# Optimization experiments

Measured on AMD Instinct MI355X. Metric: run time of the kernel, lower is better.

## Reference

```python
import jax, jax.numpy as jnp
import numpy as np

B, T, C = 4, 2048, 768
H, D = 6, 128


def apply_rotary_emb(x, cos, sin):
    # x: (B, T, H, D); cos, sin: (1, T, 1, D//2)
    d = x.shape[-1] // 2
    x1, x2 = x[..., :d], x[..., d:]
    y1 = x1 * cos + x2 * sin
    y2 = -x1 * sin + x2 * cos
    return jnp.concatenate([y1, y2], axis=-1)


def rmsnorm(x):
    eps = 1e-15
    ms = jnp.mean(x * x, axis=-1, keepdims=True)
    return x / jnp.sqrt(ms + eps)


def setup_inputs() -> dict:
    key = jax.random.key(0)
    ks = jax.random.split(key, 7)
    s = 0.02
    return {
        "x": jax.random.normal(ks[0], (B, T, C), jnp.float32),
        "cos": jax.random.normal(ks[1], (1, T, 1, D // 2), jnp.float32),
        "sin": jax.random.normal(ks[2], (1, T, 1, D // 2), jnp.float32),
        "Wq": jax.random.normal(ks[3], (C, C), jnp.float32) * s,
        "Wk": jax.random.normal(ks[4], (C, C), jnp.float32) * s,
        "Wv": jax.random.normal(ks[5], (C, C), jnp.float32) * s,
        "Wo": jax.random.normal(ks[6], (C, C), jnp.float32) * s,
    }


def reference(x, cos, sin, Wq, Wk, Wv, Wo):
    b, t, c = x.shape
    # QKV projections (nn.Linear: x @ W.T)
    q = (x @ Wq.T).reshape(b, t, H, D)
    k = (x @ Wk.T).reshape(b, t, H, D)
    v = (x @ Wv.T).reshape(b, t, H, D)
    # RoPE then QK-RMSNorm
    q = rmsnorm(apply_rotary_emb(q, cos, sin))
    k = rmsnorm(apply_rotary_emb(k, cos, sin))
    # (B, H, T, D)
    q = q.transpose(0, 2, 1, 3)
    k = k.transpose(0, 2, 1, 3)
    v = v.transpose(0, 2, 1, 3)
    scores = jnp.einsum('bhqd,bhkd->bhqk', q, k) / jnp.sqrt(jnp.float32(D))
    causal = jnp.tril(jnp.ones((t, t), dtype=bool))
    scores = jnp.where(causal[None, None], scores, -jnp.inf)
    attn = jax.nn.softmax(scores, axis=-1)
    out = jnp.einsum('bhqk,bhkd->bhqd', attn, v)
    out = out.transpose(0, 2, 1, 3).reshape(b, t, c)
    return out @ Wo.T
```

## Files before the change

### kernel.cpp

```cpp
#include <hip/hip_runtime.h>

#define T_SEQ 2048
#define NH    6
#define HD    128
#define CDIM  768
#define NQKV  2304
#define MROWS 8192
#define NSLOT 1920

typedef __attribute__((ext_vector_type(8))) short bf16x8;
typedef __attribute__((ext_vector_type(4))) float f32x4;

__device__ __forceinline__ unsigned short f2bf(float f){
  unsigned int u = __builtin_bit_cast(unsigned int, f);
  u += 0x7fffu + ((u >> 16) & 1u);
  return (unsigned short)(u >> 16);
}
__device__ __forceinline__ float bf2f(unsigned short h){
  unsigned int u = ((unsigned int)h) << 16;
  return __builtin_bit_cast(float, u);
}

__device__ __forceinline__ void gload_lds16(const void* g, void* l){
  __builtin_amdgcn_global_load_lds(
      (const __attribute__((address_space(1))) unsigned int*)g,
      (__attribute__((address_space(3))) unsigned int*)l, 16, 0, 0);
}

__device__ __forceinline__ int offq(int q){
  return q < 8 ? q : q < 16 ? 8 + 2*(q-8) : q < 24 ? 24 + 3*(q-16) : 48 + 4*(q-24);
}

__global__ __launch_bounds__(256) void cvt_f32_bf16(
    const float* __restrict__ in, unsigned short* __restrict__ out, int n4){
  int i = blockIdx.x * 256 + threadIdx.x;
  if (i >= n4) return;
  float4 v = reinterpret_cast<const float4*>(in)[i];
  ushort4 o;
  o.x = f2bf(v.x); o.y = f2bf(v.y); o.z = f2bf(v.z); o.w = f2bf(v.w);
  reinterpret_cast<ushort4*>(out)[i] = o;
}

__global__ __launch_bounds__(256) void cvt_w4(
    const float* __restrict__ w0, const float* __restrict__ w1,
    const float* __restrict__ w2, const float* __restrict__ w3,
    unsigned short* __restrict__ out){
  const int which = blockIdx.y;
  const float* src = which == 0 ? w0 : which == 1 ? w1 : which == 2 ? w2 : w3;
  int i = blockIdx.x * 256 + threadIdx.x;
  float4 v = reinterpret_cast<const float4*>(src)[i];
  ushort4 o;
  o.x = f2bf(v.x); o.y = f2bf(v.y); o.z = f2bf(v.z); o.w = f2bf(v.w);
  reinterpret_cast<ushort4*>(out + (size_t)which * CDIM * CDIM)[i] = o;
}

template<int BF16OUT>
__global__ __launch_bounds__(256) void gemm_bt(
    const unsigned short* __restrict__ A,
    const unsigned short* __restrict__ B,
    void* __restrict__ Cv, int M, int N, int K)
{
  __shared__ unsigned short As[128 * 64];
  __shared__ unsigned short Bs[128 * 64];
  const int tid  = threadIdx.x;
  const int lane = tid & 63;
  const int wave = tid >> 6;
  const int wm = wave >> 1, wn = wave & 1;
  const int lr = lane & 15, lg = lane >> 4;
  const int srow = lane >> 3;
  const int sslot = (lane & 7) ^ (lane >> 3);
  const int row0 = blockIdx.x * 128, col0 = blockIdx.y * 128;

  f32x4 acc[4][4];
  const f32x4 z = {0.f, 0.f, 0.f, 0.f};
  #pragma unroll
  for (int i = 0; i < 4; ++i)
    #pragma unroll
    for (int j = 0; j < 4; ++j) acc[i][j] = z;

  for (int k0 = 0; k0 < K; k0 += 64){
    #pragma unroll
    for (int i = 0; i < 4; ++i){
      int seg = wave * 4 + i;
      int r = seg * 8 + srow;
      gload_lds16(&A[(size_t)(row0 + r) * K + k0 + sslot * 8], &As[seg * 512]);
      gload_lds16(&B[(size_t)(col0 + r) * K + k0 + sslot * 8], &Bs[seg * 512]);
    }
    __syncthreads();
    #pragma unroll
    for (int kk = 0; kk < 64; kk += 32){
      bf16x8 af[4], bfr[4];
      #pragma unroll
      for (int mi = 0; mi < 4; ++mi)
        af[mi] = *reinterpret_cast<const bf16x8*>(
            &As[(wm*64 + mi*16 + lr) * 64 + ((((kk>>3) + lg) ^ (lr & 7)) * 8)]);
      #pragma unroll
      for (int ni = 0; ni < 4; ++ni)
        bfr[ni] = *reinterpret_cast<const bf16x8*>(
            &Bs[(wn*64 + ni*16 + lr) * 64 + ((((kk>>3) + lg) ^ (lr & 7)) * 8)]);
      #pragma unroll
      for (int mi = 0; mi < 4; ++mi)
        #pragma unroll
        for (int ni = 0; ni < 4; ++ni)
          acc[mi][ni] = __builtin_amdgcn_mfma_f32_16x16x32_bf16(af[mi], bfr[ni], acc[mi][ni], 0, 0, 0);
    }
    __syncthreads();
  }
  #pragma unroll
  for (int mi = 0; mi < 4; ++mi){
    #pragma unroll
    for (int ni = 0; ni < 4; ++ni){
      #pragma unroll
      for (int r = 0; r < 4; ++r){
        int row = row0 + wm*64 + mi*16 + lg*4 + r;
        int col = col0 + wn*64 + ni*16 + lr;
        if (BF16OUT)
          reinterpret_cast<unsigned short*>(Cv)[(size_t)row * N + col] = f2bf(acc[mi][ni][r]);
        else
          reinterpret_cast<float*>(Cv)[(size_t)row * N + col] = acc[mi][ni][r];
      }
    }
  }
}

__global__ __launch_bounds__(256) void rope_rms(
    unsigned short* __restrict__ QKVb,
    const float* __restrict__ cosp, const float* __restrict__ sinp)
{
  const int bt    = blockIdx.x;
  const int task  = blockIdx.y * 4 + (threadIdx.x >> 6);
  const int which = task / NH;
  const int h     = task % NH;
  const int t     = bt & (T_SEQ - 1);
  const int lane  = threadIdx.x & 63;
  unsigned short* p = QKVb + (size_t)bt * NQKV + which * CDIM + h * HD;
  float x1 = bf2f(p[lane]);
  float x2 = bf2f(p[lane + 64]);
  float c = cosp[t * 64 + lane];
  float s = sinp[t * 64 + lane];
  float y1 = x1 * c + x2 * s;
  float y2 = x2 * c - x1 * s;
  float ss = y1 * y1 + y2 * y2;
  #pragma unroll
  for (int off = 1; off < 64; off <<= 1) ss += __shfl_xor(ss, off);
  float inv = rsqrtf(ss * (1.0f / 128.0f) + 1e-15f);
  p[lane]      = f2bf(y1 * inv);
  p[lane + 64] = f2bf(y2 * inv);
}

__global__ __launch_bounds__(256) void transpose_v(
    const unsigned short* __restrict__ QKVb, unsigned short* __restrict__ Vt)
{
  __shared__ unsigned short tile[64][66];
  const int tid = threadIdx.x;
  const int t0  = blockIdx.x * 64;
  const int hd  = blockIdx.y;
  const int b   = blockIdx.z;
  const int h = hd >> 1, dhalf = (hd & 1) * 64;
  const unsigned short* src = QKVb + (size_t)b * T_SEQ * NQKV + 2 * CDIM + h * HD + dhalf;
  #pragma unroll
  for (int it = 0; it < 2; ++it){
    int ch = tid + it * 256;
    int r = ch >> 3, cc = (ch & 7) * 8;
    *reinterpret_cast<int4*>(&tile[r][cc]) =
        *reinterpret_cast<const int4*>(&src[(size_t)(t0 + r) * NQKV + cc]);
  }
  __syncthreads();
  unsigned short* dst = Vt + ((size_t)(b * NH + h) * HD + dhalf) * T_SEQ + t0;
  #pragma unroll
  for (int it = 0; it < 2; ++it){
    int ch = tid + it * 256;
    int d = ch >> 3, cc = (ch & 7) * 8;
    union { int4 v; unsigned short u[8]; } w;
    #pragma unroll
    for (int j = 0; j < 8; ++j) w.u[j] = tile[cc + j][d];
    *reinterpret_cast<int4*>(&dst[(size_t)d * T_SEQ + cc]) = w.v;
  }
}

__global__ __launch_bounds__(256) void attn_fwd(
    const unsigned short* __restrict__ QKVb,
    const unsigned short* __restrict__ Vt,
    unsigned short* __restrict__ AO,
    float* __restrict__ Op, float* __restrict__ Mp, float* __restrict__ Lp,
    int split)
{
  __shared__ unsigned short Ks[64][136];
  __shared__ unsigned short Vs[128][72];
  const int tid = threadIdx.x;
  const int lane = tid & 63, wave = tid >> 6;
  const int lr = lane & 15, lg = lane >> 4;
  float* Ps = reinterpret_cast<float*>(&Ks[0][0]) + wave * 1024;

  const int bh = blockIdx.y;
  const int b = bh / NH, h = bh % NH;
  int q, c, nc;
  if (split){
    int L = blockIdx.x;
    if (L < 8)      { q = L; c = 0; }
    else if (L < 24){ int m = L - 8;  q = 8 + (m >> 1); c = m & 1; }
    else if (L < 48){ int m = L - 24; q = 16 + m / 3;   c = m % 3; }
    else            { int m = L - 48; q = 24 + (m >> 2); c = m & 3; }
    nc = (q + 8) >> 3;
  } else { q = blockIdx.x; c = 0; nc = 1; }
  const int q0 = q * 64;
  const int qw = q0 + wave * 16;
  const int tbeg = c * 8;
  const int tend = split ? ((tbeg + 8 < q + 1) ? tbeg + 8 : q + 1) : q + 1;

  const unsigned short* Qp = QKVb + (size_t)(b * T_SEQ) * NQKV + h * HD;
  const unsigned short* Kp = QKVb + (size_t)(b * T_SEQ) * NQKV + CDIM + h * HD;
  const unsigned short* Vp = Vt + (size_t)bh * HD * T_SEQ;

  bf16x8 qf[4];
  #pragma unroll
  for (int c4 = 0; c4 < 4; ++c4)
    qf[c4] = *reinterpret_cast<const bf16x8*>(&Qp[(size_t)(qw + lr) * NQKV + c4 * 32 + lg * 8]);

  const f32x4 z = {0.f, 0.f, 0.f, 0.f};
  f32x4 o[8];
  #pragma unroll
  for (int dt = 0; dt < 8; ++dt) o[dt] = z;
  float mrun[4], lrun[4];
  #pragma unroll
  for (int r = 0; r < 4; ++r){ mrun[r] = -__builtin_inff(); lrun[r] = 0.f; }
  const float scl = 0.08838834764831845f;

  for (int t = tbeg; t < tend; ++t){
    const int kv0 = t * 64;
    #pragma unroll
    for (int it = 0; it < 4; ++it){
      int ch = tid + it * 256;
      int r = ch >> 4, cc = (ch & 15) * 8;
      *reinterpret_cast<int4*>(&Ks[r][cc]) =
          *reinterpret_cast<const int4*>(&Kp[(size_t)(kv0 + r) * NQKV + cc]);
      int rv = ch >> 3, cv = (ch & 7) * 8;
      *reinterpret_cast<int4*>(&Vs[rv][cv]) =
          *reinterpret_cast<const int4*>(&Vp[(size_t)rv * T_SEQ + kv0 + cv]);
    }
    __syncthreads();

    f32x4 s[4];
    #pragma unroll
    for (int nt = 0; nt < 4; ++nt) s[nt] = z;
    __builtin_amdgcn_s_setprio(1);
    #pragma unroll
    for (int c4 = 0; c4 < 4; ++c4){
      #pragma unroll
      for (int nt = 0; nt < 4; ++nt){
        bf16x8 kf = *reinterpret_cast<const bf16x8*>(&Ks[nt * 16 + lr][c4 * 32 + lg * 8]);
        s[nt] = __builtin_amdgcn_mfma_f32_16x16x32_bf16(qf[c4], kf, s[nt], 0, 0, 0);
      }
    }
    __builtin_amdgcn_s_setprio(0);
    __syncthreads();

    if (kv0 + 63 > qw){
      #pragma unroll
      for (int nt = 0; nt < 4; ++nt){
        int kg = kv0 + nt * 16 + lr;
        #pragma unroll
        for (int r = 0; r < 4; ++r){
          int qg = qw + lg * 4 + r;
          s[nt][r] = (kg <= qg) ? s[nt][r] * scl : -__builtin_inff();
        }
      }
    } else {
      #pragma unroll
      for (int nt = 0; nt < 4; ++nt)
        #pragma unroll
        for (int r = 0; r < 4; ++r) s[nt][r] *= scl;
    }

    float pm[4], rs[4];
    #pragma unroll
    for (int r = 0; r < 4; ++r)
      pm[r] = fmaxf(fmaxf(s[0][r], s[1][r]), fmaxf(s[2][r], s[3][r]));
    #pragma unroll
    for (int off = 1; off < 16; off <<= 1){
      #pragma unroll
      for (int r = 0; r < 4; ++r) pm[r] = fmaxf(pm[r], __shfl_xor(pm[r], off));
    }
    bool grow = false;
    #pragma unroll
    for (int r = 0; r < 4; ++r) grow = grow || (pm[r] > mrun[r]);
    if (__any(grow)){
      float sc[4];
      #pragma unroll
      for (int r = 0; r < 4; ++r){
        float mn = fmaxf(mrun[r], pm[r]);
        sc[r] = (mrun[r] == -__builtin_inff()) ? 0.f : __expf(mrun[r] - mn);
        mrun[r] = mn;
      }
      #pragma unroll
      for (int r = 0; r < 4; ++r) lrun[r] *= sc[r];
      #pragma unroll
      for (int dt = 0; dt < 8; ++dt)
        #pragma unroll
        for (int r = 0; r < 4; ++r) o[dt][r] *= sc[r];
    }
    #pragma unroll
    for (int r = 0; r < 4; ++r) rs[r] = 0.f;
    #pragma unroll
    for (int nt = 0; nt < 4; ++nt)
      #pragma unroll
      for (int r = 0; r < 4; ++r){
        float p = __expf(s[nt][r] - mrun[r]);
        s[nt][r] = p;
        rs[r] += p;
      }
    #pragma unroll
    for (int off = 1; off < 16; off <<= 1){
      #pragma unroll
      for (int r = 0; r < 4; ++r) rs[r] += __shfl_xor(rs[r], off);
    }
    #pragma unroll
    for (int r = 0; r < 4; ++r) lrun[r] += rs[r];

    #pragma unroll
    for (int nt = 0; nt < 4; ++nt)
      #pragma unroll
      for (int r = 0; r < 4; ++r){
        int row = lg * 4 + r;
        Ps[row * 64 + ((nt * 16 + lr) ^ ((row & 7) << 2))] = s[nt][r];
      }

    __builtin_amdgcn_s_setprio(1);
    #pragma unroll
    for (int kc = 0; kc < 2; ++kc){
      float4 p0 = *reinterpret_cast<const float4*>(
          &Ps[lr * 64 + ((kc * 32 + lg * 8) ^ ((lr & 7) << 2))]);
      float4 p1 = *reinterpret_cast<const float4*>(
          &Ps[lr * 64 + (((kc * 32 + lg * 8) + 4) ^ ((lr & 7) << 2))]);
      union { bf16x8 v; unsigned short u[8]; } pa;
      pa.u[0] = f2bf(p0.x); pa.u[1] = f2bf(p0.y); pa.u[2] = f2bf(p0.z); pa.u[3] = f2bf(p0.w);
      pa.u[4] = f2bf(p1.x); pa.u[5] = f2bf(p1.y); pa.u[6] = f2bf(p1.z); pa.u[7] = f2bf(p1.w);
      #pragma unroll
      for (int dt = 0; dt < 8; ++dt){
        bf16x8 vf = *reinterpret_cast<const bf16x8*>(&Vs[dt * 16 + lr][kc * 32 + lg * 8]);
        o[dt] = __builtin_amdgcn_mfma_f32_16x16x32_bf16(pa.v, vf, o[dt], 0, 0, 0);
      }
    }
    __builtin_amdgcn_s_setprio(0);
    __syncthreads();
  }

  if (nc == 1){
    float inv[4];
    #pragma unroll
    for (int r = 0; r < 4; ++r) inv[r] = 1.0f / lrun[r];
    #pragma unroll
    for (int dt = 0; dt < 8; ++dt)
      #pragma unroll
      for (int r = 0; r < 4; ++r)
        AO[((size_t)b * T_SEQ + qw + lg * 4 + r) * CDIM + h * HD + dt * 16 + lr] =
            f2bf(o[dt][r] * inv[r]);
  } else {
    const int slot = bh * 80 + offq(q) + c;
    float* OpW = Op + (size_t)slot * 64 * 128;
    #pragma unroll
    for (int dt = 0; dt < 8; ++dt)
      #pragma unroll
      for (int r = 0; r < 4; ++r)
        OpW[(wave * 16 + lg * 4 + r) * 128 + dt * 16 + lr] = o[dt][r];
    if (lr == 0){
      #pragma unroll
      for (int r = 0; r < 4; ++r){
        int row = wave * 16 + lg * 4 + r;
        Mp[(size_t)slot * 64 + row] = mrun[r];
        Lp[(size_t)slot * 64 + row] = lrun[r];
      }
    }
  }
}

__global__ __launch_bounds__(256) void attn_combine(
    const float* __restrict__ Op, const float* __restrict__ Mp,
    const float* __restrict__ Lp, unsigned short* __restrict__ AO)
{
  const int q  = 8 + blockIdx.x;
  const int bh = blockIdx.y;
  const int b = bh / NH, h = bh % NH;
  const int nc = (q + 8) >> 3;
  const int slot0 = bh * 80 + offq(q);
  #pragma unroll
  for (int u = 0; u < 8; ++u){
    int unit = threadIdx.x + u * 256;
    int r = unit >> 5, d4 = unit & 31;
    float m = -__builtin_inff();
    for (int cc = 0; cc < nc; ++cc)
      m = fmaxf(m, Mp[(size_t)(slot0 + cc) * 64 + r]);
    float l = 0.f;
    float a0 = 0.f, a1 = 0.f, a2 = 0.f, a3 = 0.f;
    for (int cc = 0; cc < nc; ++cc){
      float w = __expf(Mp[(size_t)(slot0 + cc) * 64 + r] - m);
      l += w * Lp[(size_t)(slot0 + cc) * 64 + r];
      const float4 v = *reinterpret_cast<const float4*>(
          &Op[((size_t)(slot0 + cc) * 64 + r) * 128 + d4 * 4]);
      a0 += w * v.x; a1 += w * v.y; a2 += w * v.z; a3 += w * v.w;
    }
    float inv = 1.0f / l;
    ushort4 ov;
    ov.x = f2bf(a0 * inv); ov.y = f2bf(a1 * inv);
    ov.z = f2bf(a2 * inv); ov.w = f2bf(a3 * inv);
    *reinterpret_cast<ushort4*>(
        &AO[((size_t)b * T_SEQ + q * 64 + r) * CDIM + h * HD + d4 * 4]) = ov;
  }
}

extern "C" void kernel_launch(void* const* d_in, const int* in_sizes, int n_in,
                              void* d_out, int out_size, void* d_ws, size_t ws_size,
                              hipStream_t stream)
{
  (void)in_sizes; (void)n_in; (void)out_size;
  const float* x    = (const float*)d_in[0];
  const float* cosp = (const float*)d_in[1];
  const float* sinp = (const float*)d_in[2];
  const float* Wq   = (const float*)d_in[3];
  const float* Wk   = (const float*)d_in[4];
  const float* Wv   = (const float*)d_in[5];
  const float* Wo   = (const float*)d_in[6];
  float* out = (float*)d_out;

  unsigned short* xb    = (unsigned short*)d_ws;
  unsigned short* Wqkvb = xb    + (size_t)MROWS * CDIM;
  unsigned short* Wob   = Wqkvb + (size_t)NQKV * CDIM;
  unsigned short* QKVb  = Wob   + (size_t)CDIM * CDIM;
  unsigned short* Vtb   = QKVb  + (size_t)MROWS * NQKV;
  unsigned short* AO    = Vtb   + (size_t)MROWS * CDIM;
  float* Op = (float*)(AO + (size_t)MROWS * CDIM);
  float* Mp = Op + (size_t)NSLOT * 64 * 128;
  float* Lp = Mp + (size_t)NSLOT * 64;
  size_t need = (size_t)((char*)(Lp + (size_t)NSLOT * 64) - (char*)d_ws);
  const int split = (ws_size >= need) ? 1 : 0;

  int n4x = MROWS * CDIM / 4;
  cvt_f32_bf16<<<(n4x + 255) / 256, 256, 0, stream>>>(x, xb, n4x);
  cvt_w4<<<dim3(CDIM * CDIM / 4 / 256, 4), 256, 0, stream>>>(Wq, Wk, Wv, Wo, Wqkvb);

  gemm_bt<1><<<dim3(MROWS / 128, NQKV / 128), 256, 0, stream>>>(xb, Wqkvb, QKVb, MROWS, NQKV, CDIM);
  rope_rms<<<dim3(MROWS, 3), 256, 0, stream>>>(QKVb, cosp, sinp);
  transpose_v<<<dim3(T_SEQ / 64, 12, 4), 256, 0, stream>>>(QKVb, Vtb);
  attn_fwd<<<dim3(split ? 80 : 32, 4 * NH), 256, 0, stream>>>(
      QKVb, Vtb, AO, Op, Mp, Lp, split);
  if (split)
    attn_combine<<<dim3(24, 24), 256, 0, stream>>>(Op, Mp, Lp, AO);
  gemm_bt<0><<<dim3(MROWS / 128, CDIM / 128), 256, 0, stream>>>(AO, Wob, out, MROWS, CDIM, CDIM);
}
```

Baseline: 217.7 us.

## Remap workgroups for XCD locality, schedule heavy attention tiles first, bf16 partials

GEMM workgroups are remapped so consecutive tiles land on the same XCD (a chiplet-aware swizzle), which aims to improve L2 reuse. The attention launch becomes a flat grid that is XCD-swizzled and reversed so the longest causal tiles start first, which aims to reduce tail imbalance. The split-K partial outputs are now stored in bf16 instead of fp32, roughly halving combine traffic at some cost in precision. The P-matrix bf16 conversion uses the packed v_cvt_pk_bf16_f32 instruction.

```diff
diff --git a/kernel.cpp b/kernel.cpp
--- a/kernel.cpp
+++ b/kernel.cpp
@@ -19,6 +19,11 @@
 __device__ __forceinline__ float bf2f(unsigned short h){
   unsigned int u = ((unsigned int)h) << 16;
   return __builtin_bit_cast(float, u);
+}
+__device__ __forceinline__ unsigned int cvtpk(float lo, float hi){
+  unsigned int r;
+  asm("v_cvt_pk_bf16_f32 %0, %1, %2" : "=v"(r) : "v"(lo), "v"(hi));
+  return r;
 }
 
 __device__ __forceinline__ void gload_lds16(const void* g, void* l){
@@ -69,7 +74,10 @@
   const int lr = lane & 15, lg = lane >> 4;
   const int srow = lane >> 3;
   const int sslot = (lane & 7) ^ (lane >> 3);
-  const int row0 = blockIdx.x * 128, col0 = blockIdx.y * 128;
+  const int gx = gridDim.x, nwg = gx * gridDim.y;
+  const int flat = blockIdx.y * gx + blockIdx.x;
+  const int nf = (flat & 7) * (nwg >> 3) + (flat >> 3);
+  const int row0 = (nf % gx) * 128, col0 = (nf / gx) * 128;
 
   f32x4 acc[4][4];
   const f32x4 z = {0.f, 0.f, 0.f, 0.f};
@@ -182,7 +190,7 @@
     const unsigned short* __restrict__ QKVb,
     const unsigned short* __restrict__ Vt,
     unsigned short* __restrict__ AO,
-    float* __restrict__ Op, float* __restrict__ Mp, float* __restrict__ Lp,
+    unsigned short* __restrict__ Op, float* __restrict__ Mp, float* __restrict__ Lp,
     int split)
 {
   __shared__ unsigned short Ks[64][136];
@@ -192,17 +200,19 @@
   const int lr = lane & 15, lg = lane >> 4;
   float* Ps = reinterpret_cast<float*>(&Ks[0][0]) + wave * 1024;
 
-  const int bh = blockIdx.y;
-  const int b = bh / NH, h = bh % NH;
-  int q, c, nc;
+  int bh, q, c, nc;
   if (split){
-    int L = blockIdx.x;
+    const int flat = blockIdx.x;
+    const int nf = (flat & 7) * 240 + (flat >> 3);
+    bh = nf / 80;
+    const int L = 79 - (nf % 80);
     if (L < 8)      { q = L; c = 0; }
     else if (L < 24){ int m = L - 8;  q = 8 + (m >> 1); c = m & 1; }
     else if (L < 48){ int m = L - 24; q = 16 + m / 3;   c = m % 3; }
     else            { int m = L - 48; q = 24 + (m >> 2); c = m & 3; }
     nc = (q + 8) >> 3;
-  } else { q = blockIdx.x; c = 0; nc = 1; }
+  } else { bh = blockIdx.y; q = blockIdx.x; c = 0; nc = 1; }
+  const int b = bh / NH, h = bh % NH;
   const int q0 = q * 64;
   const int qw = q0 + wave * 16;
   const int tbeg = c * 8;
@@ -332,9 +342,9 @@
           &Ps[lr * 64 + ((kc * 32 + lg * 8) ^ ((lr & 7) << 2))]);
       float4 p1 = *reinterpret_cast<const float4*>(
           &Ps[lr * 64 + (((kc * 32 + lg * 8) + 4) ^ ((lr & 7) << 2))]);
-      union { bf16x8 v; unsigned short u[8]; } pa;
-      pa.u[0] = f2bf(p0.x); pa.u[1] = f2bf(p0.y); pa.u[2] = f2bf(p0.z); pa.u[3] = f2bf(p0.w);
-      pa.u[4] = f2bf(p1.x); pa.u[5] = f2bf(p1.y); pa.u[6] = f2bf(p1.z); pa.u[7] = f2bf(p1.w);
+      union { bf16x8 v; unsigned int u[4]; } pa;
+      pa.u[0] = cvtpk(p0.x, p0.y); pa.u[1] = cvtpk(p0.z, p0.w);
+      pa.u[2] = cvtpk(p1.x, p1.y); pa.u[3] = cvtpk(p1.z, p1.w);
       #pragma unroll
       for (int dt = 0; dt < 8; ++dt){
         bf16x8 vf = *reinterpret_cast<const bf16x8*>(&Vs[dt * 16 + lr][kc * 32 + lg * 8]);
@@ -357,12 +367,12 @@
             f2bf(o[dt][r] * inv[r]);
   } else {
     const int slot = bh * 80 + offq(q) + c;
-    float* OpW = Op + (size_t)slot * 64 * 128;
+    unsigned short* OpW = Op + (size_t)slot * 64 * 128;
     #pragma unroll
     for (int dt = 0; dt < 8; ++dt)
       #pragma unroll
       for (int r = 0; r < 4; ++r)
-        OpW[(wave * 16 + lg * 4 + r) * 128 + dt * 16 + lr] = o[dt][r];
+        OpW[(wave * 16 + lg * 4 + r) * 128 + dt * 16 + lr] = f2bf(o[dt][r]);
     if (lr == 0){
       #pragma unroll
       for (int r = 0; r < 4; ++r){
@@ -375,7 +385,7 @@
 }
 
 __global__ __launch_bounds__(256) void attn_combine(
-    const float* __restrict__ Op, const float* __restrict__ Mp,
+    const unsigned short* __restrict__ Op, const float* __restrict__ Mp,
     const float* __restrict__ Lp, unsigned short* __restrict__ AO)
 {
   const int q  = 8 + blockIdx.x;
@@ -395,9 +405,10 @@
     for (int cc = 0; cc < nc; ++cc){
       float w = __expf(Mp[(size_t)(slot0 + cc) * 64 + r] - m);
       l += w * Lp[(size_t)(slot0 + cc) * 64 + r];
-      const float4 v = *reinterpret_cast<const float4*>(
+      const ushort4 v = *reinterpret_cast<const ushort4*>(
           &Op[((size_t)(slot0 + cc) * 64 + r) * 128 + d4 * 4]);
-      a0 += w * v.x; a1 += w * v.y; a2 += w * v.z; a3 += w * v.w;
+      a0 += w * bf2f(v.x); a1 += w * bf2f(v.y);
+      a2 += w * bf2f(v.z); a3 += w * bf2f(v.w);
     }
     float inv = 1.0f / l;
     ushort4 ov;
@@ -428,8 +439,8 @@
   unsigned short* QKVb  = Wob   + (size_t)CDIM * CDIM;
   unsigned short* Vtb   = QKVb  + (size_t)MROWS * NQKV;
   unsigned short* AO    = Vtb   + (size_t)MROWS * CDIM;
-  float* Op = (float*)(AO + (size_t)MROWS * CDIM);
-  float* Mp = Op + (size_t)NSLOT * 64 * 128;
+  unsigned short* Op    = AO    + (size_t)MROWS * CDIM;
+  float* Mp = (float*)(Op + (size_t)NSLOT * 64 * 128);
   float* Lp = Mp + (size_t)NSLOT * 64;
   size_t need = (size_t)((char*)(Lp + (size_t)NSLOT * 64) - (char*)d_ws);
   const int split = (ws_size >= need) ? 1 : 0;
@@ -441,8 +452,10 @@
   gemm_bt<1><<<dim3(MROWS / 128, NQKV / 128), 256, 0, stream>>>(xb, Wqkvb, QKVb, MROWS, NQKV, CDIM);
   rope_rms<<<dim3(MROWS, 3), 256, 0, stream>>>(QKVb, cosp, sinp);
   transpose_v<<<dim3(T_SEQ / 64, 12, 4), 256, 0, stream>>>(QKVb, Vtb);
-  attn_fwd<<<dim3(split ? 80 : 32, 4 * NH), 256, 0, stream>>>(
-      QKVb, Vtb, AO, Op, Mp, Lp, split);
+  if (split)
+    attn_fwd<<<1920, 256, 0, stream>>>(QKVb, Vtb, AO, Op, Mp, Lp, 1);
+  else
+    attn_fwd<<<dim3(32, 24), 256, 0, stream>>>(QKVb, Vtb, AO, Op, Mp, Lp, 0);
   if (split)
     attn_combine<<<dim3(24, 24), 256, 0, stream>>>(Op, Mp, Lp, AO);
   gemm_bt<0><<<dim3(MROWS / 128, CDIM / 128), 256, 0, stream>>>(AO, Wob, out, MROWS, CDIM, CDIM);
```

Result: slower. 222.9 us (+2.4%).
